# Optimization experiments

Hardware: AMD Instinct MI355X
Metric: run time of the kernel (lower is better)

## Reference

```python
import jax, jax.numpy as jnp
import numpy as np

B, N, C, NH = 8, 16384, 256, 8
CH = C // NH          # head dim = 32
SCALE = CH ** -0.5
HH = WW = 128         # N = HH*WW
# CoaT crpe window dict {3:2, 5:3, 7:3}: 2 heads->3x3, 3 heads->5x5, 3 heads->7x7


def setup_inputs() -> dict:
    key = jax.random.key(0)
    ks = jax.random.split(key, 9)
    w = lambda k, shp: (jax.random.normal(k, shp, jnp.float32) * 0.02)
    return {
        "x": jax.random.normal(ks[0], (B, N, C), jnp.float32),
        "w_qkv": w(ks[1], (C, 3 * C)),              # qkv_bias=False
        "w_proj": w(ks[2], (C, C)),
        "b_proj": jnp.zeros((C,), jnp.float32),
        "w3": w(ks[3], (3, 3, 1, 2 * CH)),          # HWIO depthwise, 2 heads
        "b3": jnp.zeros((2 * CH,), jnp.float32),
        "w5": w(ks[4], (5, 5, 1, 3 * CH)),          # 3 heads
        "b5": jnp.zeros((3 * CH,), jnp.float32),
        "w7": w(ks[5], (7, 7, 1, 3 * CH)),          # 3 heads
        "b7": jnp.zeros((3 * CH,), jnp.float32),
        "H": HH,
        "W": WW,
    }


def _hydra(q, k, v):
    # q,k,v: [B, h, N, Ch]; normalize over feature dim, O(N) token reduction
    qn = q * jax.lax.rsqrt(jnp.sum(q * q, axis=-1, keepdims=True))
    kn = k * jax.lax.rsqrt(jnp.sum(k * k, axis=-1, keepdims=True))
    kv = jnp.sum(kn * v, axis=-2, keepdims=True)   # [B, h, 1, Ch]
    return qn * kv                                  # broadcast over tokens


def _dwconv(img, kern, bias):
    # img: [B, c, H, W]; kern: [kh, kw, 1, c] (HWIO depthwise)
    c = img.shape[1]
    out = jax.lax.conv_general_dilated(
        img, kern, window_strides=(1, 1), padding="SAME",
        feature_group_count=c,
        dimension_numbers=("NCHW", "HWIO", "NCHW"))
    return out + bias[None, :, None, None]


def _crpe(q, v, Hs, Ws, convs):
    # CoaT ConvRelPosEnc: depthwise conv on v per head group, gated by q
    b, h, n, ch = v.shape
    outs, idx = [], 0
    for heads, kern, bias in convs:
        vs = v[:, idx:idx + heads]                          # [B, hs, N, Ch]
        v_img = vs.transpose(0, 1, 3, 2).reshape(b, heads * ch, Hs, Ws)
        cv = _dwconv(v_img, kern, bias)
        cv = cv.reshape(b, heads, ch, n).transpose(0, 1, 3, 2)
        outs.append(q[:, idx:idx + heads] * cv)
        idx += heads
    return jnp.concatenate(outs, axis=1)                    # [B, h, N, Ch]


def reference(x, w_qkv, w_proj, b_proj, w3, b3, w5, b5, w7, b7, H, W):
    b, n, c = x.shape
    qkv = (x @ w_qkv).reshape(b, n, 3, NH, CH).transpose(2, 0, 3, 1, 4)
    q, k, v = qkv[0], qkv[1], qkv[2]                        # [B, h, N, Ch]
    factor_att = _hydra(q, k, v)
    crpe = _crpe(q, v, H, W, [(2, w3, b3), (3, w5, b5), (3, w7, b7)])
    out = SCALE * factor_att + crpe
    out = out.transpose(0, 2, 1, 3).reshape(b, n, c)        # [B, N, C]
    return out @ w_proj + b_proj
```

## Files before the change

kernel.cpp:

```cpp
#include <hip/hip_runtime.h>
#include <hip/hip_bf16.h>


typedef __hip_bfloat16 bf16;
typedef __bf16 bf16x8 __attribute__((ext_vector_type(8)));
typedef unsigned short u16x8 __attribute__((ext_vector_type(8)));
typedef float f32x4 __attribute__((ext_vector_type(4)));
typedef float f32x8 __attribute__((ext_vector_type(8)));

#define SCALE_ 0.17677669529663687f

__device__ __forceinline__ unsigned short f2b(float f) {
  __hip_bfloat16 h = __float2bfloat16(f);
  return __builtin_bit_cast(unsigned short, h);
}
__device__ __forceinline__ float blo(unsigned u) {
  return __builtin_bit_cast(float, u << 16);
}
__device__ __forceinline__ float bhi(unsigned u) {
  return __builtin_bit_cast(float, u & 0xffff0000u);
}
__device__ __forceinline__ f32x8 unpack8(uint4 u) {
  f32x8 r;
  r[0] = blo(u.x); r[1] = bhi(u.x); r[2] = blo(u.y); r[3] = bhi(u.y);
  r[4] = blo(u.z); r[5] = bhi(u.z); r[6] = blo(u.w); r[7] = bhi(u.w);
  return r;
}
__device__ __forceinline__ uint4 pack8v(const f32x8 o) {
  uint4 s;
  s.x = (unsigned)f2b(o[0]) | ((unsigned)f2b(o[1]) << 16);
  s.y = (unsigned)f2b(o[2]) | ((unsigned)f2b(o[3]) << 16);
  s.z = (unsigned)f2b(o[4]) | ((unsigned)f2b(o[5]) << 16);
  s.w = (unsigned)f2b(o[6]) | ((unsigned)f2b(o[7]) << 16);
  return s;
}
__device__ __forceinline__ void gload16(const void* g, void* l) {
  __builtin_amdgcn_global_load_lds(
      (const __attribute__((address_space(1))) unsigned int*)g,
      (__attribute__((address_space(3))) unsigned int*)l, 16, 0, 0);
}
__device__ __forceinline__ f32x4 mfma16(u16x8 a, u16x8 b, f32x4 c) {
  return __builtin_amdgcn_mfma_f32_16x16x32_bf16(
      __builtin_bit_cast(bf16x8, a), __builtin_bit_cast(bf16x8, b), c, 0, 0, 0);
}
__device__ __forceinline__ void barrier_vm4() {
  asm volatile("s_waitcnt vmcnt(4) lgkmcnt(0)" ::: "memory");
  __builtin_amdgcn_s_barrier();
  asm volatile("" ::: "memory");
}
__device__ __forceinline__ void barrier_vm0() {
  asm volatile("s_waitcnt vmcnt(0) lgkmcnt(0)" ::: "memory");
  __builtin_amdgcn_s_barrier();
  asm volatile("" ::: "memory");
}
__device__ __forceinline__ void fma8(f32x8& a, const f32x8 v, const float4 w0,
                                     const float4 w1) {
  a[0] += v[0] * w0.x; a[1] += v[1] * w0.y;
  a[2] += v[2] * w0.z; a[3] += v[3] * w0.w;
  a[4] += v[4] * w1.x; a[5] += v[5] * w1.y;
  a[6] += v[6] * w1.z; a[7] += v[7] * w1.w;
}

__global__ __launch_bounds__(256) void prep_weights(
    const float* __restrict__ wqkv, const float* __restrict__ wproj,
    bf16* __restrict__ wqkvT, bf16* __restrict__ wprojT) {
  const int idx = blockIdx.x * 256 + threadIdx.x;
  if (idx < 768 * 256) {
    const int j = idx >> 8, k = idx & 255;
    wqkvT[idx] = __float2bfloat16(wqkv[k * 768 + j]);
  }
  if (idx < 256 * 256) {
    const int j = idx >> 8, k = idx & 255;
    wprojT[idx] = __float2bfloat16(wproj[k * 256 + j]);
  }
}

__global__ __launch_bounds__(256) void prep_x(const float* __restrict__ x,
                                              bf16* __restrict__ xb) {
  const size_t idx = ((size_t)blockIdx.x * 256 + threadIdx.x) * 8;
  const float4 a0 = *(const float4*)(x + idx);
  const float4 a1 = *(const float4*)(x + idx + 4);
  u16x8 p;
  p[0] = f2b(a0.x); p[1] = f2b(a0.y); p[2] = f2b(a0.z); p[3] = f2b(a0.w);
  p[4] = f2b(a1.x); p[5] = f2b(a1.y); p[6] = f2b(a1.z); p[7] = f2b(a1.w);
  *(u16x8*)(xb + idx) = p;
}

__global__ __launch_bounds__(256) void qkv_mfma(
    const bf16* __restrict__ xb, const bf16* __restrict__ wT,
    bf16* __restrict__ qO, bf16* __restrict__ kO, bf16* __restrict__ vO) {
  __shared__ __align__(16) char LDSU[49152];
  char* As = LDSU;
  char* Bs = LDSU + 24576;
  const int tid = threadIdx.x;
  const int l = tid & 63, w = tid >> 6;
  const int wr = w >> 1, wc = w & 1;

  const int lin = blockIdx.y * 6 + blockIdx.x;
  const int xcd = lin & 7, qq = lin >> 3;
  const int jt = qq % 6;
  const int ttile = xcd * 128 + qq / 6;
  const int j0 = jt << 7;
  const int t0 = ttile << 7;
  const int b = t0 >> 14;
  const int n0 = t0 & 16383;

  f32x4 acc[4][4];
#pragma unroll
  for (int m = 0; m < 4; ++m)
#pragma unroll
    for (int t = 0; t < 4; ++t) acc[m][t] = (f32x4){0.f, 0.f, 0.f, 0.f};

  const int row0 = w * 16 + (l >> 2), row1 = row0 + 64;
  const int sl = l & 3;
  const int sw0 = (row0 >> 1) & 3, sw1 = (row1 >> 1) & 3;
  const bf16* asrc0 = wT + (size_t)(j0 + row0) * 256 + ((sl ^ sw0) << 3);
  const bf16* asrc1 = wT + (size_t)(j0 + row1) * 256 + ((sl ^ sw1) << 3);
  const bf16* bsrc0 = xb + (size_t)(t0 + row0) * 256 + ((sl ^ sw0) << 3);
  const bf16* bsrc1 = xb + (size_t)(t0 + row1) * 256 + ((sl ^ sw1) << 3);
  const int d0 = w * 1024, d1 = 4096 + w * 1024;

  const int fr = l & 15;
  const int fq = l >> 4;
  const int fs = (fq ^ ((l >> 1) & 3)) << 4;

  gload16(asrc0, As + d0);
  gload16(asrc1, As + d1);
  gload16(bsrc0, Bs + d0);
  gload16(bsrc1, Bs + d1);
  gload16(asrc0 + 32, As + 8192 + d0);
  gload16(asrc1 + 32, As + 8192 + d1);
  gload16(bsrc0 + 32, Bs + 8192 + d0);
  gload16(bsrc1 + 32, Bs + 8192 + d1);
  barrier_vm4();

#pragma unroll
  for (int t = 0; t < 8; ++t) {
    if (t < 6) {
      const int kn = (t + 2) << 5;
      const int nb = ((t + 2) % 3) * 8192;
      gload16(asrc0 + kn, As + nb + d0);
      gload16(asrc1 + kn, As + nb + d1);
      gload16(bsrc0 + kn, Bs + nb + d0);
      gload16(bsrc1 + kn, Bs + nb + d1);
    }
    const char* Ac = As + (t % 3) * 8192;
    const char* Bc = Bs + (t % 3) * 8192;
    u16x8 af[4], bfv[4];
#pragma unroll
    for (int m = 0; m < 4; ++m)
      af[m] = *(const u16x8*)(Ac + (wr * 64 + m * 16 + fr) * 64 + fs);
#pragma unroll
    for (int tt = 0; tt < 4; ++tt)
      bfv[tt] = *(const u16x8*)(Bc + (wc * 64 + tt * 16 + fr) * 64 + fs);
    __builtin_amdgcn_s_setprio(1);
#pragma unroll
    for (int m = 0; m < 4; ++m)
#pragma unroll
      for (int tt = 0; tt < 4; ++tt)
        acc[m][tt] = mfma16(af[m], bfv[tt], acc[m][tt]);
    __builtin_amdgcn_s_setprio(0);
    if (t < 6) barrier_vm4();
    else if (t < 7) barrier_vm0();
  }
  __syncthreads();

#pragma unroll
  for (int m = 0; m < 4; ++m) {
    const int jq = wr * 16 + m * 4 + fq;
#pragma unroll
    for (int t = 0; t < 4; ++t) {
      const int token = wc * 64 + t * 16 + fr;
      const int p = jq ^ (token & 15);
      uint2 pk;
      pk.x = (unsigned)f2b(acc[m][t][0]) | ((unsigned)f2b(acc[m][t][1]) << 16);
      pk.y = (unsigned)f2b(acc[m][t][2]) | ((unsigned)f2b(acc[m][t][3]) << 16);
      *(uint2*)(LDSU + token * 256 + (p << 3)) = pk;
    }
  }
  __syncthreads();

  const int region = j0 >> 8;
  bf16* outp = (region == 0) ? qO : ((region == 1) ? kO : vO);
  const int jl = j0 & 255;
  const int seg = tid & 15;
#pragma unroll
  for (int r = 0; r < 8; ++r) {
    const int token = r * 16 + (tid >> 4);
    const int tsw = token & 15;
    const uint2 lo = *(const uint2*)(LDSU + token * 256 + (((2 * seg) ^ tsw) << 3));
    const uint2 hi =
        *(const uint2*)(LDSU + token * 256 + (((2 * seg + 1) ^ tsw) << 3));
    uint4 d;
    d.x = lo.x; d.y = lo.y; d.z = hi.x; d.w = hi.y;
    *(uint4*)&outp[((size_t)b * 16384 + n0 + token) * 256 + jl + seg * 8] = d;
  }
}

__global__ __launch_bounds__(256) void kv_reduce(
    const bf16* __restrict__ kT, const bf16* __restrict__ vT,
    float* __restrict__ kv) {
  __shared__ float red[256 * 8];
  const int tid = threadIdx.x;
  const int b = blockIdx.y;
  const int seg = tid & 31;
  f32x8 part = (f32x8)0.f;

  for (int r = 0; r < 32; ++r) {
    const int token = blockIdx.x * 256 + r * 8 + (tid >> 5);
    const size_t roff = ((size_t)b * 16384 + token) * 256;
    const uint4 kd = *(const uint4*)(kT + roff + seg * 8);
    const f32x8 kf = unpack8(kd);
    float ss = 0.f;
#pragma unroll
    for (int i = 0; i < 8; ++i) ss += kf[i] * kf[i];
    ss += __shfl_xor(ss, 1);
    ss += __shfl_xor(ss, 2);
    const float inv = rsqrtf(ss);
    const uint4 vd = *(const uint4*)(vT + roff + seg * 8);
    const f32x8 vf = unpack8(vd);
#pragma unroll
    for (int i = 0; i < 8; ++i) part[i] += kf[i] * inv * vf[i];
  }
#pragma unroll
  for (int i = 0; i < 8; ++i) red[tid * 8 + i] = part[i];
  __syncthreads();
  if (tid < 32) {
    f32x8 s = (f32x8)0.f;
#pragma unroll
    for (int k = 0; k < 8; ++k)
#pragma unroll
      for (int i = 0; i < 8; ++i) s[i] += red[(tid + 32 * k) * 8 + i];
#pragma unroll
    for (int i = 0; i < 8; ++i)
      atomicAdd(&kv[b * 256 + seg * 8 + i], s[i]);
  }
}

template <int K>
__global__ __launch_bounds__(256) void crpe_conv(
    const bf16* __restrict__ qT, const bf16* __restrict__ vT,
    const float* __restrict__ kvbuf, const float* __restrict__ wp,
    const float* __restrict__ bp, int OC, int hbase,
    bf16* __restrict__ mid) {
  constexpr int R = K / 2;
  constexpr int SY = 16 + 2 * R;
  constexpr int SXr = 32 + 2 * R;
  constexpr int SX = SXr + 1;
  constexpr int PL = SX * SY;
  __shared__ __align__(16) uint4 vs[4 * PL];
  __shared__ float wlds[K * K * 32];
  __shared__ float blds[32];

  const int tid = threadIdx.x;
  const int hg = blockIdx.x;
  const int h = hbase + hg;
  const int tile = blockIdx.y;
  const int b = blockIdx.z;
  const int tx0 = (tile & 3) * 32, ty0 = (tile >> 2) * 16;
  const int tx = tid & 15, ty = tid >> 4;
  const int ocbase = hg * 32;

  {
    const int cc = tid & 3;
    for (int e = tid >> 2; e < SXr * SY; e += 64) {
      const int ly = e / SXr, lx = e - ly * SXr;
      const int gy = ty0 - R + ly, gx = tx0 - R + lx;
      uint4 d = {0, 0, 0, 0};
      if (gy >= 0 && gy < 128 && gx >= 0 && gx < 128)
        d = *((const uint4*)(vT + ((size_t)b * 16384 + gy * 128 + gx) * 256 +
                             h * 32) + cc);
      vs[cc * PL + ly * SX + lx] = d;
    }
  }
  for (int e = tid; e < K * K * 32; e += 256)
    wlds[e] = wp[(e >> 5) * OC + ocbase + (e & 31)];
  if (tid < 32) blds[tid] = bp[ocbase + tid];
  __syncthreads();

  const int n = (ty0 + ty) * 128 + tx0 + 2 * tx;
  const size_t off0 = ((size_t)b * 16384 + n) * 256 + h * 32;
  const uint4* q0 = (const uint4*)(qT + off0);
  const uint4* q1 = (const uint4*)(qT + off0 + 256);
  float ss0 = 0.f, ss1 = 0.f;
#pragma unroll
  for (int cc = 0; cc < 4; ++cc) {
    const f32x8 a = unpack8(q0[cc]);
    const f32x8 c = unpack8(q1[cc]);
#pragma unroll
    for (int i = 0; i < 8; ++i) { ss0 += a[i] * a[i]; ss1 += c[i] * c[i]; }
  }
  const float qinv0 = rsqrtf(ss0), qinv1 = rsqrtf(ss1);
  const float4* kvp = (const float4*)(kvbuf + ((size_t)b * 8 + h) * 32);
  const float4* wlds4 = (const float4*)wlds;
  const float4* bl4 = (const float4*)blds;
  uint4* m0 = (uint4*)(mid + off0);
  uint4* m1 = (uint4*)(mid + off0 + 256);

#pragma unroll 1
  for (int cc = 0; cc < 4; ++cc) {
    const uint4* vplane = vs + cc * PL;
    const float4 ba = bl4[cc * 2], bb = bl4[cc * 2 + 1];
    f32x8 a0, a1;
    a0[0] = ba.x; a0[1] = ba.y; a0[2] = ba.z; a0[3] = ba.w;
    a0[4] = bb.x; a0[5] = bb.y; a0[6] = bb.z; a0[7] = bb.w;
    a1 = a0;
#pragma unroll
    for (int ky = 0; ky < K; ++ky) {
      const uint4* vrow = vplane + (ty + ky) * SX + 2 * tx;
      f32x8 vcur = unpack8(vrow[0]);
#pragma unroll
      for (int kx = 0; kx < K; ++kx) {
        const f32x8 vnx = unpack8(vrow[kx + 1]);
        const float4 w0 = wlds4[(ky * K + kx) * 8 + cc * 2];
        const float4 w1 = wlds4[(ky * K + kx) * 8 + cc * 2 + 1];
        fma8(a0, vcur, w0, w1);
        fma8(a1, vnx, w0, w1);
        vcur = vnx;
      }
    }
    const float4 ka = kvp[cc * 2], kb = kvp[cc * 2 + 1];
    f32x8 kvf;
    kvf[0] = ka.x; kvf[1] = ka.y; kvf[2] = ka.z; kvf[3] = ka.w;
    kvf[4] = kb.x; kvf[5] = kb.y; kvf[6] = kb.z; kvf[7] = kb.w;
    {
      const f32x8 qv = unpack8(q0[cc]);
      f32x8 o;
#pragma unroll
      for (int i = 0; i < 8; ++i)
        o[i] = SCALE_ * qv[i] * qinv0 * kvf[i] + qv[i] * a0[i];
      m0[cc] = pack8v(o);
    }
    {
      const f32x8 qv = unpack8(q1[cc]);
      f32x8 o;
#pragma unroll
      for (int i = 0; i < 8; ++i)
        o[i] = SCALE_ * qv[i] * qinv1 * kvf[i] + qv[i] * a1[i];
      m1[cc] = pack8v(o);
    }
  }
}

__global__ __launch_bounds__(256) void proj_mfma(
    const bf16* __restrict__ mid, const bf16* __restrict__ wpT,
    const float* __restrict__ bproj, float* __restrict__ out) {
  __shared__ __align__(16) char LDSU[49152];
  char* As = LDSU;
  char* Bs = LDSU + 24576;
  const int tid = threadIdx.x;
  const int l = tid & 63, w = tid >> 6;
  const int wr = w >> 1, wc = w & 1;

  const int lin = blockIdx.y * 2 + blockIdx.x;
  const int xcd = lin & 7, qq = lin >> 3;
  const int jt = qq & 1;
  const int ttile = xcd * 128 + (qq >> 1);
  const int j0 = jt << 7;
  const int tk0 = ttile << 7;

  f32x4 acc[4][4];
#pragma unroll
  for (int m = 0; m < 4; ++m)
#pragma unroll
    for (int t = 0; t < 4; ++t) acc[m][t] = (f32x4){0.f, 0.f, 0.f, 0.f};

  const int row0 = w * 16 + (l >> 2), row1 = row0 + 64;
  const int sl = l & 3;
  const int sw0 = (row0 >> 1) & 3, sw1 = (row1 >> 1) & 3;
  const bf16* asrc0 = wpT + (size_t)(j0 + row0) * 256 + ((sl ^ sw0) << 3);
  const bf16* asrc1 = wpT + (size_t)(j0 + row1) * 256 + ((sl ^ sw1) << 3);
  const bf16* bsrc0 = mid + (size_t)(tk0 + row0) * 256 + ((sl ^ sw0) << 3);
  const bf16* bsrc1 = mid + (size_t)(tk0 + row1) * 256 + ((sl ^ sw1) << 3);
  const int d0 = w * 1024, d1 = 4096 + w * 1024;

  const int fr = l & 15;
  const int fq = l >> 4;
  const int fs = (fq ^ ((l >> 1) & 3)) << 4;

  gload16(asrc0, As + d0);
  gload16(asrc1, As + d1);
  gload16(bsrc0, Bs + d0);
  gload16(bsrc1, Bs + d1);
  gload16(asrc0 + 32, As + 8192 + d0);
  gload16(asrc1 + 32, As + 8192 + d1);
  gload16(bsrc0 + 32, Bs + 8192 + d0);
  gload16(bsrc1 + 32, Bs + 8192 + d1);
  barrier_vm4();

#pragma unroll
  for (int t = 0; t < 8; ++t) {
    if (t < 6) {
      const int kn = (t + 2) << 5;
      const int nb = ((t + 2) % 3) * 8192;
      gload16(asrc0 + kn, As + nb + d0);
      gload16(asrc1 + kn, As + nb + d1);
      gload16(bsrc0 + kn, Bs + nb + d0);
      gload16(bsrc1 + kn, Bs + nb + d1);
    }
    const char* Ac = As + (t % 3) * 8192;
    const char* Bc = Bs + (t % 3) * 8192;
    u16x8 af[4], bfv[4];
#pragma unroll
    for (int m = 0; m < 4; ++m)
      af[m] = *(const u16x8*)(Ac + (wr * 64 + m * 16 + fr) * 64 + fs);
#pragma unroll
    for (int tt = 0; tt < 4; ++tt)
      bfv[tt] = *(const u16x8*)(Bc + (wc * 64 + tt * 16 + fr) * 64 + fs);
    __builtin_amdgcn_s_setprio(1);
#pragma unroll
    for (int m = 0; m < 4; ++m)
#pragma unroll
      for (int tt = 0; tt < 4; ++tt)
        acc[m][tt] = mfma16(af[m], bfv[tt], acc[m][tt]);
    __builtin_amdgcn_s_setprio(0);
    if (t < 6) barrier_vm4();
    else if (t < 7) barrier_vm0();
  }
  __syncthreads();

#pragma unroll
  for (int m = 0; m < 4; ++m) {
    const float4 bias = *(const float4*)&bproj[j0 + wr * 64 + m * 16 + fq * 4];
#pragma unroll
    for (int t = 0; t < 4; ++t) {
      acc[m][t][0] += bias.x;
      acc[m][t][1] += bias.y;
      acc[m][t][2] += bias.z;
      acc[m][t][3] += bias.w;
    }
  }

  for (int chunk = 0; chunk < 2; ++chunk) {
    if (wc == chunk) {
#pragma unroll
      for (int m = 0; m < 4; ++m) {
        const int jq = wr * 16 + m * 4 + fq;
#pragma unroll
        for (int t = 0; t < 4; ++t) {
          const int ltok = t * 16 + fr;
          const int p = jq ^ (ltok & 15);
          float4 r;
          r.x = acc[m][t][0]; r.y = acc[m][t][1];
          r.z = acc[m][t][2]; r.w = acc[m][t][3];
          *(float4*)(LDSU + ltok * 512 + (p << 4)) = r;
        }
      }
    }
    __syncthreads();
    const int seg = tid & 31;
#pragma unroll
    for (int r = 0; r < 8; ++r) {
      const int ltok = r * 8 + (tid >> 5);
      const int p = seg ^ (ltok & 15);
      const float4 dv = *(const float4*)(LDSU + ltok * 512 + (p << 4));
      *(float4*)&out[(size_t)(tk0 + chunk * 64 + ltok) * 256 + j0 + seg * 4] = dv;
    }
    __syncthreads();
  }
}

extern "C" void kernel_launch(void* const* d_in, const int* in_sizes, int n_in,
                              void* d_out, int out_size, void* d_ws,
                              size_t ws_size, hipStream_t stream) {
  const float* x     = (const float*)d_in[0];
  const float* wqkv  = (const float*)d_in[1];
  const float* wproj = (const float*)d_in[2];
  const float* bproj = (const float*)d_in[3];
  const float* w3 = (const float*)d_in[4];
  const float* b3 = (const float*)d_in[5];
  const float* w5 = (const float*)d_in[6];
  const float* b5 = (const float*)d_in[7];
  const float* w7 = (const float*)d_in[8];
  const float* b7 = (const float*)d_in[9];
  float* out = (float*)d_out;

  const size_t PLANE = (size_t)8 * 16384 * 256;
  bf16* qT  = (bf16*)d_ws;
  bf16* vT  = qT + PLANE;
  bf16* kT  = vT + PLANE;
  bf16* mid = kT;
  float* kv = (float*)(kT + PLANE);
  bf16* wqkvT  = (bf16*)(kv + 2048);
  bf16* wprojT = wqkvT + 768 * 256;
  bf16* xb = (bf16*)d_out;

  hipMemsetAsync(kv, 0, 2048 * sizeof(float), stream);
  prep_weights<<<dim3(768), 256, 0, stream>>>(wqkv, wproj, wqkvT, wprojT);
  prep_x<<<dim3(16384), 256, 0, stream>>>(x, xb);
  qkv_mfma<<<dim3(6, 1024), 256, 0, stream>>>(xb, wqkvT, qT, kT, vT);
  kv_reduce<<<dim3(64, 8), 256, 0, stream>>>(kT, vT, kv);
  crpe_conv<3><<<dim3(2, 32, 8), 256, 0, stream>>>(qT, vT, kv, w3, b3, 64, 0, mid);
  crpe_conv<5><<<dim3(3, 32, 8), 256, 0, stream>>>(qT, vT, kv, w5, b5, 96, 2, mid);
  crpe_conv<7><<<dim3(3, 32, 8), 256, 0, stream>>>(qT, vT, kv, w7, b7, 96, 5, mid);
  proj_mfma<<<dim3(2, 1024), 256, 0, stream>>>(mid, wprojT, bproj, out);
}
```

Measured before the change: 353.9 us.

## Merge prep kernels, widen kv_reduce grid, stage crpe output through LDS

Three changes are bundled. The x-conversion and weight-transpose kernels are merged into one launch. kv_reduce now uses four times as many blocks, each covering 64 tokens instead of 256, to raise parallelism at the cost of more atomic partial reductions. crpe_conv now holds its outputs in registers, writes them to a swizzled LDS tile, and then stores them to global memory in a coalesced pattern. That replaces the scattered per-thread 64-byte stores but adds two barriers and more register pressure.

```diff
diff --git a/kernel.cpp b/kernel.cpp
--- a/kernel.cpp
+++ b/kernel.cpp
@@ -61,29 +61,30 @@
   a[6] += v[6] * w1.z; a[7] += v[7] * w1.w;
 }
 
-__global__ __launch_bounds__(256) void prep_weights(
-    const float* __restrict__ wqkv, const float* __restrict__ wproj,
+__global__ __launch_bounds__(256) void prep_all(
+    const float* __restrict__ x, const float* __restrict__ wqkv,
+    const float* __restrict__ wproj, bf16* __restrict__ xb,
     bf16* __restrict__ wqkvT, bf16* __restrict__ wprojT) {
-  const int idx = blockIdx.x * 256 + threadIdx.x;
-  if (idx < 768 * 256) {
-    const int j = idx >> 8, k = idx & 255;
-    wqkvT[idx] = __float2bfloat16(wqkv[k * 768 + j]);
-  }
-  if (idx < 256 * 256) {
-    const int j = idx >> 8, k = idx & 255;
-    wprojT[idx] = __float2bfloat16(wproj[k * 256 + j]);
-  }
-}
-
-__global__ __launch_bounds__(256) void prep_x(const float* __restrict__ x,
-                                              bf16* __restrict__ xb) {
-  const size_t idx = ((size_t)blockIdx.x * 256 + threadIdx.x) * 8;
-  const float4 a0 = *(const float4*)(x + idx);
-  const float4 a1 = *(const float4*)(x + idx + 4);
-  u16x8 p;
-  p[0] = f2b(a0.x); p[1] = f2b(a0.y); p[2] = f2b(a0.z); p[3] = f2b(a0.w);
-  p[4] = f2b(a1.x); p[5] = f2b(a1.y); p[6] = f2b(a1.z); p[7] = f2b(a1.w);
-  *(u16x8*)(xb + idx) = p;
+  const int bid = blockIdx.x;
+  if (bid < 16384) {
+    const size_t idx = ((size_t)bid * 256 + threadIdx.x) * 8;
+    const float4 a0 = *(const float4*)(x + idx);
+    const float4 a1 = *(const float4*)(x + idx + 4);
+    u16x8 p;
+    p[0] = f2b(a0.x); p[1] = f2b(a0.y); p[2] = f2b(a0.z); p[3] = f2b(a0.w);
+    p[4] = f2b(a1.x); p[5] = f2b(a1.y); p[6] = f2b(a1.z); p[7] = f2b(a1.w);
+    *(u16x8*)(xb + idx) = p;
+  } else {
+    const int idx = (bid - 16384) * 256 + threadIdx.x;
+    if (idx < 768 * 256) {
+      const int j = idx >> 8, k = idx & 255;
+      wqkvT[idx] = __float2bfloat16(wqkv[k * 768 + j]);
+    }
+    if (idx < 256 * 256) {
+      const int j = idx >> 8, k = idx & 255;
+      wprojT[idx] = __float2bfloat16(wproj[k * 256 + j]);
+    }
+  }
 }
 
 __global__ __launch_bounds__(256) void qkv_mfma(
@@ -206,8 +207,8 @@
   const int seg = tid & 31;
   f32x8 part = (f32x8)0.f;
 
-  for (int r = 0; r < 32; ++r) {
-    const int token = blockIdx.x * 256 + r * 8 + (tid >> 5);
+  for (int r = 0; r < 8; ++r) {
+    const int token = blockIdx.x * 64 + r * 8 + (tid >> 5);
     const size_t roff = ((size_t)b * 16384 + token) * 256;
     const uint4 kd = *(const uint4*)(kT + roff + seg * 8);
     const f32x8 kf = unpack8(kd);
@@ -294,10 +295,9 @@
   const float4* kvp = (const float4*)(kvbuf + ((size_t)b * 8 + h) * 32);
   const float4* wlds4 = (const float4*)wlds;
   const float4* bl4 = (const float4*)blds;
-  uint4* m0 = (uint4*)(mid + off0);
-  uint4* m1 = (uint4*)(mid + off0 + 256);
-
-#pragma unroll 1
+
+  uint4 po0[4], po1[4];
+#pragma unroll
   for (int cc = 0; cc < 4; ++cc) {
     const uint4* vplane = vs + cc * PL;
     const float4 ba = bl4[cc * 2], bb = bl4[cc * 2 + 1];
@@ -329,7 +329,7 @@
 #pragma unroll
       for (int i = 0; i < 8; ++i)
         o[i] = SCALE_ * qv[i] * qinv0 * kvf[i] + qv[i] * a0[i];
-      m0[cc] = pack8v(o);
+      po0[cc] = pack8v(o);
     }
     {
       const f32x8 qv = unpack8(q1[cc]);
@@ -337,8 +337,27 @@
 #pragma unroll
       for (int i = 0; i < 8; ++i)
         o[i] = SCALE_ * qv[i] * qinv1 * kvf[i] + qv[i] * a1[i];
-      m1[cc] = pack8v(o);
-    }
+      po1[cc] = pack8v(o);
+    }
+  }
+
+  __syncthreads();
+  const int p0 = ty * 32 + 2 * tx, p1 = p0 + 1;
+#pragma unroll
+  for (int cc = 0; cc < 4; ++cc) {
+    vs[p0 * 4 + (cc ^ (p0 & 3))] = po0[cc];
+    vs[p1 * 4 + (cc ^ (p1 & 3))] = po1[cc];
+  }
+  __syncthreads();
+  const size_t tbase = ((size_t)b * 16384) * 256 + h * 32;
+#pragma unroll
+  for (int r = 0; r < 8; ++r) {
+    const int gid = r * 256 + tid;
+    const int px = gid >> 2, cc = gid & 3;
+    const int py = px >> 5, pxx = px & 31;
+    const int nn = (ty0 + py) * 128 + tx0 + pxx;
+    const uint4 d = vs[px * 4 + (cc ^ (px & 3))];
+    *((uint4*)(mid + tbase + (size_t)nn * 256) + cc) = d;
   }
 }
 
@@ -486,10 +505,10 @@
   bf16* xb = (bf16*)d_out;
 
   hipMemsetAsync(kv, 0, 2048 * sizeof(float), stream);
-  prep_weights<<<dim3(768), 256, 0, stream>>>(wqkv, wproj, wqkvT, wprojT);
-  prep_x<<<dim3(16384), 256, 0, stream>>>(x, xb);
+  prep_all<<<dim3(16384 + 768), 256, 0, stream>>>(x, wqkv, wproj, xb, wqkvT,
+                                                  wprojT);
   qkv_mfma<<<dim3(6, 1024), 256, 0, stream>>>(xb, wqkvT, qT, kT, vT);
-  kv_reduce<<<dim3(64, 8), 256, 0, stream>>>(kT, vT, kv);
+  kv_reduce<<<dim3(256, 8), 256, 0, stream>>>(kT, vT, kv);
   crpe_conv<3><<<dim3(2, 32, 8), 256, 0, stream>>>(qT, vT, kv, w3, b3, 64, 0, mid);
   crpe_conv<5><<<dim3(3, 32, 8), 256, 0, stream>>>(qT, vT, kv, w5, b5, 96, 2, mid);
   crpe_conv<7><<<dim3(3, 32, 8), 256, 0, stream>>>(qT, vT, kv, w7, b7, 96, 5, mid);
```

Result: slower. 400.1 us (+13.1%).
